# Optimization experiments

Measured on AMD Instinct MI355X. Metric: run time of the kernel, lower is better.

The kernel has to match this reference:

```python
import jax, jax.numpy as jnp
import numpy as np

N_HEAD = 8
N_HB_TERM = 3


def setup_inputs() -> dict:
    key = jax.random.key(0)
    ks = jax.random.split(key, 6)
    B, N, C, T = 8, 4096, 512, 4096
    s = 0.02  # weight init scale
    return {
        "x": jax.random.normal(ks[0], (B, N, C), jnp.float32),
        "y": jax.random.normal(ks[1], (N_HB_TERM, B, T, C), jnp.float32),
        "Wq": jax.random.normal(ks[2], (C, C), jnp.float32) * s,
        "bq": jnp.zeros((C,), jnp.float32),
        "Wk": jax.random.normal(ks[3], (N_HB_TERM, C, C), jnp.float32) * s,
        "bk": jnp.zeros((N_HB_TERM, C), jnp.float32),
        "Wv": jax.random.normal(ks[4], (N_HB_TERM, C, C), jnp.float32) * s,
        "bv": jnp.zeros((N_HB_TERM, C), jnp.float32),
        "Wp": jax.random.normal(ks[5], (C, C), jnp.float32) * s,
        "bp": jnp.zeros((C,), jnp.float32),
    }


def _heads(t, B, T, H, d):
    # (B, T, C) -> (B, H, T, d)
    return t.reshape(B, T, H, d).transpose(0, 2, 1, 3)


def reference(x, y, Wq, bq, Wk, bk, Wv, bv, Wp, bp):
    B, N, C = x.shape
    H = N_HEAD
    d = C // H
    # query projection + softmax feature map over head dim
    q = _heads(x @ Wq.T + bq, B, N, H, d)          # (B,H,N,d)
    q = jax.nn.softmax(q, axis=-1)
    out = q  # faithful to original: out initialized to q
    for i in range(N_HB_TERM):
        yi = y[i]                                   # (B,T,C)
        T = yi.shape[1]
        k = _heads(yi @ Wk[i].T + bk[i], B, T, H, d)
        v = _heads(yi @ Wv[i].T + bv[i], B, T, H, d)
        k = jax.nn.softmax(k, axis=-1)
        k_cumsum = k.sum(axis=-2, keepdims=True)    # (B,H,1,d)
        D_inv = 1.0 / (q * k_cumsum).sum(axis=-1, keepdims=True)  # (B,H,N,1)
        ctx = jnp.einsum('bhtd,bhte->bhde', k, v)   # (B,H,d,d) small context
        out = out + jnp.einsum('bhnd,bhde->bhne', q, ctx) * D_inv
    out = out.transpose(0, 2, 1, 3).reshape(B, N, C)  # b h n d -> b n (h d)
    return out @ Wp.T + bp
```

## Files before the change

kernel.cpp:

```cpp
#include <hip/hip_runtime.h>


#define B_  8
#define N_  4096
#define C_  512
#define T_  4096
#define H_  8
#define M_  (B_*N_)

typedef __bf16 bf16_8 __attribute__((ext_vector_type(8)));
typedef __bf16 bf16_4 __attribute__((ext_vector_type(4)));
typedef float  f32_4  __attribute__((ext_vector_type(4)));

__device__ __forceinline__ unsigned short f2bf(float f) {
  unsigned u = __float_as_uint(f);
  unsigned r = 0x7FFFu + ((u >> 16) & 1u);
  return (unsigned short)((u + r) >> 16);
}
__device__ __forceinline__ unsigned pack2(float lo, float hi) {
  return (unsigned)f2bf(lo) | ((unsigned)f2bf(hi) << 16);
}

__device__ __forceinline__ void gload16(const void* g, void* l) {
  __builtin_amdgcn_global_load_lds(
      (const __attribute__((address_space(1))) unsigned int*)g,
      (__attribute__((address_space(3))) unsigned int*)l, 16, 0, 0);
}

__device__ __forceinline__ bf16_8 cvt8(float4 a, float4 b) {
  bf16_8 v;
  v[0]=(__bf16)a.x; v[1]=(__bf16)a.y; v[2]=(__bf16)a.z; v[3]=(__bf16)a.w;
  v[4]=(__bf16)b.x; v[5]=(__bf16)b.y; v[6]=(__bf16)b.z; v[7]=(__bf16)b.w;
  return v;
}

__global__ __launch_bounds__(256) void cvt_all(
    const float* __restrict__ Wq, const float* __restrict__ Wk,
    const float* __restrict__ Wv, const float* __restrict__ Wp,
    const float* __restrict__ y,
    unsigned short* __restrict__ wb,
    unsigned short* __restrict__ yb)
{
  const size_t WCC = (size_t)C_*C_;
  const float* src; unsigned short* dst; long n8;
  switch (blockIdx.y) {
    case 0: src = Wq; dst = wb;         n8 = WCC/8;          break;
    case 1: src = Wk; dst = wb + WCC;   n8 = 3*WCC/8;        break;
    case 2: src = Wv; dst = wb + 4*WCC; n8 = 3*WCC/8;        break;
    case 3: src = Wp; dst = wb + 7*WCC; n8 = WCC/8;          break;
    default: src = y; dst = yb;         n8 = (long)3*M_*C_/8; break;
  }
  long i = (long)blockIdx.x * blockDim.x + threadIdx.x;
  long stride = (long)gridDim.x * blockDim.x;
  for (; i < n8; i += stride) {
    float4 a = ((const float4*)src)[2*i];
    float4 b = ((const float4*)src)[2*i + 1];
    uint4 o;
    o.x = pack2(a.x, a.y); o.y = pack2(a.z, a.w);
    o.z = pack2(b.x, b.y); o.w = pack2(b.z, b.w);
    ((uint4*)dst)[i] = o;
  }
}

__global__ __launch_bounds__(256, 2) void gemm_final(
    const unsigned short* __restrict__ A,
    const unsigned short* __restrict__ Bw,
    const float* __restrict__ bias,
    float* __restrict__ Cf)
{
  __shared__ char smem[65536];
  const int tid = threadIdx.x, lane = tid & 63, wid = tid >> 6;
  const int wr = wid >> 1, wc = wid & 1;
  const int l15 = lane & 15, l16 = lane >> 4;
  const size_t row0 = (size_t)blockIdx.x * 128;
  const int col0 = blockIdx.y * 128;

  f32_4 acc[4][4] = {};

  auto stage = [&](int k0, int bsel) {
#pragma unroll
    for (int j = 0; j < 4; ++j) {
      int cc = j*256 + tid, row = cc >> 3, s = cc & 7;
      gload16(A + (row0 + row)*512 + k0 + ((s ^ (row & 7)) << 3),
              smem + bsel*16384 + (size_t)(j*256 + wid*64)*16);
      gload16(Bw + (size_t)(col0 + row)*512 + k0 + ((s ^ (row & 7)) << 3),
              smem + 32768 + bsel*16384 + (size_t)(j*256 + wid*64)*16);
    }
  };

  stage(0, 0);
  __syncthreads();
  for (int t = 0; t < 8; ++t) {
    int cur = t & 1;
    if (t < 7) stage((t+1)*64, cur ^ 1);
    const unsigned short* sA = (const unsigned short*)(smem + cur*16384);
    const unsigned short* sB = (const unsigned short*)(smem + 32768 + cur*16384);
#pragma unroll
    for (int kk = 0; kk < 64; kk += 32) {
      bf16_8 af[4], bfr[4];
#pragma unroll
      for (int mi = 0; mi < 4; ++mi) {
        int r = wr*64 + mi*16 + l15;
        int ch = (kk >> 3) + l16;
        af[mi] = *(const bf16_8*)&sA[r*64 + ((ch ^ (r & 7)) << 3)];
      }
#pragma unroll
      for (int ni = 0; ni < 4; ++ni) {
        int r = wc*64 + ni*16 + l15;
        int ch = (kk >> 3) + l16;
        bfr[ni] = *(const bf16_8*)&sB[r*64 + ((ch ^ (r & 7)) << 3)];
      }
#pragma unroll
      for (int mi = 0; mi < 4; ++mi)
#pragma unroll
        for (int ni = 0; ni < 4; ++ni)
          acc[mi][ni] = __builtin_amdgcn_mfma_f32_16x16x32_bf16(af[mi], bfr[ni], acc[mi][ni], 0, 0, 0);
    }
    __syncthreads();
  }

#pragma unroll
  for (int mi = 0; mi < 4; ++mi) {
    int rb = wr*64 + mi*16 + l16*4;
#pragma unroll
    for (int ni = 0; ni < 4; ++ni) {
      int col = col0 + wc*64 + ni*16 + l15;
      float bv = bias[col];
#pragma unroll
      for (int jj = 0; jj < 4; ++jj)
        Cf[(row0 + rb + jj)*512 + col] = acc[mi][ni][jj] + bv;
    }
  }
}

__global__ __launch_bounds__(256, 2) void mega_kernel(
    const float* __restrict__ xf,
    const unsigned short* __restrict__ wq_b, const float* __restrict__ bq,
    unsigned short* __restrict__ qb,
    const unsigned short* __restrict__ yb_all,
    const unsigned short* __restrict__ wk_all,
    const unsigned short* __restrict__ wv_all,
    const float* __restrict__ bk_all, const float* __restrict__ bv_all,
    float* __restrict__ part, float* __restrict__ kcp)
{
  __shared__ char smem[65536];
  const int tid = threadIdx.x, lane = tid & 63, wid = tid >> 6;
  const int wr = wid >> 1, wc = wid & 1;
  const int l15 = lane & 15, l16 = lane >> 4;
  const int z = blockIdx.z;

  if (z < 2) {
    const int qidx = z*512 + blockIdx.x;
    const size_t row0 = (size_t)(qidx & 255) * 128;
    const int col0 = (qidx >> 8) * 128;

    f32_4 acc[4][4] = {};
    float4 ra[4][2];

    auto load_a = [&](int k0) {
#pragma unroll
      for (int j = 0; j < 4; ++j) {
        int cc = j*256 + tid, row = cc >> 3, s = cc & 7;
        const float* src = xf + (row0 + row)*512 + k0 + s*8;
        ra[j][0] = *(const float4*)src;
        ra[j][1] = *(const float4*)(src + 4);
      }
    };
    auto write_a = [&](int bsel) {
      unsigned short* dst = (unsigned short*)smem;
#pragma unroll
      for (int j = 0; j < 4; ++j) {
        int cc = j*256 + tid, row = cc >> 3, s = cc & 7;
        *(bf16_8*)&dst[bsel*8192 + row*64 + ((s ^ (row & 7)) << 3)] = cvt8(ra[j][0], ra[j][1]);
      }
    };
    auto stage_b = [&](int k0, int bsel) {
#pragma unroll
      for (int j = 0; j < 4; ++j) {
        int cc = j*256 + tid, row = cc >> 3, s = cc & 7;
        gload16(wq_b + (size_t)(col0 + row)*512 + k0 + ((s ^ (row & 7)) << 3),
                smem + 32768 + bsel*16384 + (size_t)(j*256 + wid*64)*16);
      }
    };

    load_a(0); stage_b(0, 0); write_a(0);
    __syncthreads();
    for (int t = 0; t < 8; ++t) {
      int cur = t & 1;
      if (t < 7) { load_a((t+1)*64); stage_b((t+1)*64, cur ^ 1); }
      const unsigned short* sA = (const unsigned short*)(smem + cur*16384);
      const unsigned short* sB = (const unsigned short*)(smem + 32768 + cur*16384);
#pragma unroll
      for (int kk = 0; kk < 64; kk += 32) {
        bf16_8 af[4], bfr[4];
#pragma unroll
        for (int mi = 0; mi < 4; ++mi) {
          int r = wr*64 + mi*16 + l15;
          int ch = (kk >> 3) + l16;
          af[mi] = *(const bf16_8*)&sA[r*64 + ((ch ^ (r & 7)) << 3)];
        }
#pragma unroll
        for (int ni = 0; ni < 4; ++ni) {
          int r = wc*64 + ni*16 + l15;
          int ch = (kk >> 3) + l16;
          bfr[ni] = *(const bf16_8*)&sB[r*64 + ((ch ^ (r & 7)) << 3)];
        }
#pragma unroll
        for (int mi = 0; mi < 4; ++mi)
#pragma unroll
          for (int ni = 0; ni < 4; ++ni)
            acc[mi][ni] = __builtin_amdgcn_mfma_f32_16x16x32_bf16(af[mi], bfr[ni], acc[mi][ni], 0, 0, 0);
      }
      if (t < 7) write_a(cur ^ 1);
      __syncthreads();
    }

    float bvv[4];
#pragma unroll
    for (int ni = 0; ni < 4; ++ni) bvv[ni] = bq[col0 + wc*64 + ni*16 + l15];
    unsigned short* sE = (unsigned short*)smem;
#pragma unroll
    for (int mi = 0; mi < 4; ++mi) {
#pragma unroll
      for (int jj = 0; jj < 4; ++jj) {
        float x[4];
        float s = 0.f;
#pragma unroll
        for (int ni = 0; ni < 4; ++ni) {
          x[ni] = __expf(acc[mi][ni][jj] + bvv[ni]);
          s += x[ni];
        }
#pragma unroll
        for (int o = 8; o; o >>= 1) s += __shfl_xor(s, o);
        float inv = 1.0f / s;
        int r = wr*64 + mi*16 + l16*4 + jj;
#pragma unroll
        for (int ni = 0; ni < 4; ++ni) {
          __bf16 h = (__bf16)(x[ni] * inv);
          sE[r*136 + wc*64 + ni*16 + l15] = *(unsigned short*)&h;
        }
      }
    }
    __syncthreads();
    int r = tid >> 1, seg = tid & 1;
    unsigned short* orow = qb + (row0 + r)*512 + col0 + seg*64;
#pragma unroll
    for (int u = 0; u < 8; ++u)
      *(uint4*)(orow + u*8) = *(const uint4*)&sE[r*136 + seg*64 + u*8];
    return;
  }

  unsigned short* sKT = (unsigned short*)smem;
  unsigned short* sVT = (unsigned short*)(smem + 17408);

  const int gx = blockIdx.x, i = z - 2;
  const int h = gx >> 6, bx = gx & 63;
  const int b = bx >> 3, sub = bx & 7;
  const int bh = b*8 + h;

  const unsigned short* yb = yb_all + (size_t)i*M_*512;
  const unsigned short* Wk_b = wk_all + (size_t)i*512*512 + (size_t)h*64*512;
  const unsigned short* Wv_b = wv_all + (size_t)i*512*512 + (size_t)h*64*512;
  const float* bk = bk_all + i*512 + h*64;
  const float* bv = bv_all + i*512 + h*64;

  f32_4 cacc[2][2] = {};
  float kcp_r[4] = {0.f, 0.f, 0.f, 0.f};

  for (int chunk = 0; chunk < 4; ++chunk) {
    const size_t row0 = (size_t)bx*512 + chunk*128;
    f32_4 acc[4][4] = {};

    auto stage = [&](int k0, int bsel) {
#pragma unroll
      for (int j = 0; j < 4; ++j) {
        int cc = j*256 + tid, row = cc >> 3, s = cc & 7;
        gload16(yb + (row0 + row)*512 + k0 + ((s ^ (row & 7)) << 3),
                smem + bsel*16384 + (size_t)(j*256 + wid*64)*16);
        const unsigned short* wsrc = (j < 2)
            ? Wk_b + (size_t)row*512
            : Wv_b + (size_t)(row - 64)*512;
        gload16(wsrc + k0 + ((s ^ (row & 7)) << 3),
                smem + 32768 + bsel*16384 + (size_t)(j*256 + wid*64)*16);
      }
    };

    stage(0, 0);
    __syncthreads();
    for (int t = 0; t < 8; ++t) {
      int cur = t & 1;
      if (t < 7) stage((t+1)*64, cur ^ 1);
      const unsigned short* sA = (const unsigned short*)(smem + cur*16384);
      const unsigned short* sB = (const unsigned short*)(smem + 32768 + cur*16384);
#pragma unroll
      for (int kk = 0; kk < 64; kk += 32) {
        bf16_8 af[4], bfr[4];
#pragma unroll
        for (int mi = 0; mi < 4; ++mi) {
          int r = wr*64 + mi*16 + l15;
          int ch = (kk >> 3) + l16;
          af[mi] = *(const bf16_8*)&sA[r*64 + ((ch ^ (r & 7)) << 3)];
        }
#pragma unroll
        for (int ni = 0; ni < 4; ++ni) {
          int r = wc*64 + ni*16 + l15;
          int ch = (kk >> 3) + l16;
          bfr[ni] = *(const bf16_8*)&sB[r*64 + ((ch ^ (r & 7)) << 3)];
        }
#pragma unroll
        for (int mi = 0; mi < 4; ++mi)
#pragma unroll
          for (int ni = 0; ni < 4; ++ni)
            acc[mi][ni] = __builtin_amdgcn_mfma_f32_16x16x32_bf16(af[mi], bfr[ni], acc[mi][ni], 0, 0, 0);
      }
      __syncthreads();
    }

    if (wc == 0) {
      float bkv[4];
#pragma unroll
      for (int ni = 0; ni < 4; ++ni) bkv[ni] = bk[ni*16 + l15];
#pragma unroll
      for (int mi = 0; mi < 4; ++mi) {
        float kv[4][4];
#pragma unroll
        for (int jj = 0; jj < 4; ++jj) {
          float s = 0.f;
#pragma unroll
          for (int ni = 0; ni < 4; ++ni) {
            kv[jj][ni] = __expf(acc[mi][ni][jj] + bkv[ni]);
            s += kv[jj][ni];
          }
#pragma unroll
          for (int o = 8; o; o >>= 1) s += __shfl_xor(s, o);
          float inv = 1.0f / s;
#pragma unroll
          for (int ni = 0; ni < 4; ++ni) kv[jj][ni] *= inv;
        }
        int r0 = wr*64 + mi*16 + l16*4;
#pragma unroll
        for (int ni = 0; ni < 4; ++ni) {
          kcp_r[ni] += (kv[0][ni] + kv[1][ni]) + (kv[2][ni] + kv[3][ni]);
          bf16_4 p;
#pragma unroll
          for (int jj = 0; jj < 4; ++jj) p[jj] = (__bf16)kv[jj][ni];
          *(bf16_4*)&sKT[(ni*16 + l15)*136 + r0] = p;
        }
      }
    } else {
      float bvv[4];
#pragma unroll
      for (int ni = 0; ni < 4; ++ni) bvv[ni] = bv[ni*16 + l15];
#pragma unroll
      for (int mi = 0; mi < 4; ++mi) {
        int r0 = wr*64 + mi*16 + l16*4;
#pragma unroll
        for (int ni = 0; ni < 4; ++ni) {
          bf16_4 p;
#pragma unroll
          for (int jj = 0; jj < 4; ++jj) p[jj] = (__bf16)(acc[mi][ni][jj] + bvv[ni]);
          *(bf16_4*)&sVT[(ni*16 + l15)*136 + r0] = p;
        }
      }
    }
    __syncthreads();

#pragma unroll
    for (int ks = 0; ks < 4; ++ks) {
      bf16_8 a2[2], b2[2];
#pragma unroll
      for (int mi = 0; mi < 2; ++mi)
        a2[mi] = *(const bf16_8*)&sKT[(wr*32 + mi*16 + l15)*136 + ks*32 + l16*8];
#pragma unroll
      for (int ni = 0; ni < 2; ++ni)
        b2[ni] = *(const bf16_8*)&sVT[(wc*32 + ni*16 + l15)*136 + ks*32 + l16*8];
#pragma unroll
      for (int mi = 0; mi < 2; ++mi)
#pragma unroll
        for (int ni = 0; ni < 2; ++ni)
          cacc[mi][ni] = __builtin_amdgcn_mfma_f32_16x16x32_bf16(a2[mi], b2[ni], cacc[mi][ni], 0, 0, 0);
    }
    __syncthreads();
  }

  const size_t slot = (size_t)(i*64 + bh)*8 + sub;
  if (wc == 0) {
#pragma unroll
    for (int ni = 0; ni < 4; ++ni) {
      float s = kcp_r[ni];
      s += __shfl_xor(s, 16);
      s += __shfl_xor(s, 32);
      if (l16 == 0) kcp[(slot*2 + wr)*64 + ni*16 + l15] = s;
    }
  }
  float* pb = part + slot*4096;
#pragma unroll
  for (int mi = 0; mi < 2; ++mi)
#pragma unroll
    for (int ni = 0; ni < 2; ++ni) {
      int e0 = wr*32 + mi*16 + l16*4;
      int dv = wc*32 + ni*16 + l15;
      *(f32_4*)&pb[dv*64 + e0] = cacc[mi][ni];
    }
}

__global__ __launch_bounds__(256) void ctx_reduce(
    const float* __restrict__ part,
    const float* __restrict__ kcp,
    float* __restrict__ ctxT,
    float* __restrict__ kc)
{
  int g = blockIdx.x;
  const float* p = part + (size_t)g*8*4096;
  float* o = ctxT + (size_t)g*4096;
#pragma unroll
  for (int jj = 0; jj < 4; ++jj) {
    int j = (jj*256 + threadIdx.x)*4;
    f32_4 s = {};
#pragma unroll
    for (int r = 0; r < 8; ++r) {
      f32_4 v = *(const f32_4*)&p[(size_t)r*4096 + j];
      s[0] += v[0]; s[1] += v[1]; s[2] += v[2]; s[3] += v[3];
    }
    *(f32_4*)&o[j] = s;
  }
  if (threadIdx.x < 64) {
    const float* pk = kcp + (size_t)g*16*64;
    float s = 0.f;
#pragma unroll
    for (int r = 0; r < 16; ++r) s += pk[r*64 + threadIdx.x];
    kc[(size_t)g*64 + threadIdx.x] = s;
  }
}

__global__ __launch_bounds__(256) void combine2(
    const unsigned short* __restrict__ qb,
    const float* __restrict__ ctxT,
    const float* __restrict__ kc,
    unsigned short* __restrict__ outp)
{
  __shared__ unsigned short sQ[128*64];
  __shared__ unsigned short sB[208*72];
  __shared__ float sS[128*3];
  const int tid = threadIdx.x, lane = tid & 63, wid = tid >> 6;
  const int l15 = lane & 15, l16 = lane >> 4;
  const int bh = blockIdx.y, b = bh >> 3, h = bh & 7;
  const int n0 = blockIdx.x * 128;
  const size_t qbase = ((size_t)b*N_ + n0)*C_ + h*64;

#pragma unroll
  for (int j = 0; j < 4; ++j) {
    int c = j*256 + tid;
    int row = c >> 3, c8 = c & 7;
    gload16(qb + qbase + (size_t)row*C_ + ((c8 ^ (row & 7)) << 3),
            sQ + (size_t)(j*256 + wid*64)*8);
  }
  for (int f = tid; f < 208*64; f += 256) {
    int col = f >> 6, e = f & 63;
    float val = 0.f;
    if (col < 192)
      val = ctxT[(((size_t)(col >> 6)*64 + bh)*64 + (col & 63))*64 + e];
    else if (col < 195)
      val = kc[((size_t)(col - 192)*64 + bh)*64 + e];
    __bf16 hv = (__bf16)val;
    sB[col*72 + e] = *(unsigned short*)&hv;
  }
  __syncthreads();

  f32_4 acc[2][13] = {};
#pragma unroll
  for (int ks = 0; ks < 2; ++ks) {
    bf16_8 af[2];
#pragma unroll
    for (int mi = 0; mi < 2; ++mi) {
      int r = wid*32 + mi*16 + l15;
      int ch = ks*4 + l16;
      af[mi] = *(const bf16_8*)&sQ[r*64 + ((ch ^ (r & 7)) << 3)];
    }
#pragma unroll
    for (int ni = 0; ni < 13; ++ni) {
      bf16_8 bfr = *(const bf16_8*)&sB[(ni*16 + l15)*72 + ks*32 + l16*8];
#pragma unroll
      for (int mi = 0; mi < 2; ++mi)
        acc[mi][ni] = __builtin_amdgcn_mfma_f32_16x16x32_bf16(af[mi], bfr, acc[mi][ni], 0, 0, 0);
    }
  }

  if (l15 < 3) {
#pragma unroll
    for (int mi = 0; mi < 2; ++mi)
#pragma unroll
      for (int jj = 0; jj < 4; ++jj)
        sS[(wid*32 + mi*16 + l16*4 + jj)*3 + l15] = acc[mi][12][jj];
  }
  __syncthreads();

#pragma unroll
  for (int mi = 0; mi < 2; ++mi) {
#pragma unroll
    for (int jj = 0; jj < 4; ++jj) {
      int r = wid*32 + mi*16 + l16*4 + jj;
      float inv[3];
#pragma unroll
      for (int i = 0; i < 3; ++i) inv[i] = 1.0f / sS[r*3 + i];
#pragma unroll
      for (int ni = 0; ni < 4; ++ni) {
        int dv = ni*16 + l15;
        unsigned short qh = sQ[r*64 + ((((dv >> 3) ^ (r & 7))) << 3) + (dv & 7)];
        float val = __uint_as_float(((unsigned)qh) << 16);
#pragma unroll
        for (int i = 0; i < 3; ++i) val += acc[mi][i*4 + ni][jj] * inv[i];
        __bf16 hv = (__bf16)val;
        outp[qbase + (size_t)r*C_ + dv] = *(unsigned short*)&hv;
      }
    }
  }
}

extern "C" void kernel_launch(void* const* d_in, const int* in_sizes, int n_in,
                              void* d_out, int out_size, void* d_ws, size_t ws_size,
                              hipStream_t stream)
{
  const float* x  = (const float*)d_in[0];
  const float* y  = (const float*)d_in[1];
  const float* Wq = (const float*)d_in[2];
  const float* bq = (const float*)d_in[3];
  const float* Wk = (const float*)d_in[4];
  const float* bk = (const float*)d_in[5];
  const float* Wv = (const float*)d_in[6];
  const float* bv = (const float*)d_in[7];
  const float* Wp = (const float*)d_in[8];
  const float* bp = (const float*)d_in[9];
  float* out = (float*)d_out;
  char* ws = (char*)d_ws;

  const size_t SZ_BF = (size_t)M_ * C_ * 2;
  const size_t WCC   = (size_t)C_ * C_;

  unsigned short* yb   = (unsigned short*)(ws);
  unsigned short* qb   = (unsigned short*)(ws + 3*SZ_BF);
  unsigned short* kb   = (unsigned short*)(ws + 4*SZ_BF);
  unsigned short* wb   = (unsigned short*)(ws + 5*SZ_BF);
  unsigned short* wq_b = wb;
  unsigned short* wk_b = wb + WCC;
  unsigned short* wv_b = wb + 4*WCC;
  unsigned short* wp_b = wb + 7*WCC;
  float* ctxT = (float*)(wb + 8*WCC);
  float* kc   = ctxT + (size_t)3*64*64*64;

  float* part  = (float*)kb;
  float* kcpar = part + (size_t)192*8*4096;

  cvt_all<<<dim3(2048, 5), 256, 0, stream>>>(Wq, Wk, Wv, Wp, y, wb, yb);

  mega_kernel<<<dim3(512, 1, 5), 256, 0, stream>>>(
      x, wq_b, bq, qb, yb, wk_b, wv_b, bk, bv, part, kcpar);
  ctx_reduce<<<192, 256, 0, stream>>>(part, kcpar, ctxT, kc);

  combine2<<<dim3(32, 64), 256, 0, stream>>>(qb, ctxT, kc, kb);
  gemm_final<<<dim3(M_/128, 4), 256, 0, stream>>>(kb, wp_b, bp, out);
}
```

Baseline: 364.7 us.

## Overlap y bf16 conversion with Q projection, split K/V context kernel

Moves the large fp32-to-bf16 conversion of y out of the up-front conversion kernel and interleaves it, on alternate blocks, with the Q projection/softmax GEMM in a new kernel. The K/V context work becomes its own kernel launched afterwards. The goal is to hide the bandwidth-bound y conversion behind compute-bound Q GEMM blocks, leaving only the small weight conversion serialized. The cost is an extra kernel launch, and the K/V blocks can no longer run concurrently with the Q blocks.

Measured after the change: 376.4 us. 1.03x slower.

```diff
diff --git a/kernel.cpp b/kernel.cpp
--- a/kernel.cpp
+++ b/kernel.cpp
@@ -34,65 +34,94 @@
   return v;
 }
 
-__global__ __launch_bounds__(256) void cvt_all(
+__global__ __launch_bounds__(256) void cvt_weights(
     const float* __restrict__ Wq, const float* __restrict__ Wk,
     const float* __restrict__ Wv, const float* __restrict__ Wp,
-    const float* __restrict__ y,
-    unsigned short* __restrict__ wb,
-    unsigned short* __restrict__ yb)
+    unsigned short* __restrict__ wb)
 {
   const size_t WCC = (size_t)C_*C_;
-  const float* src; unsigned short* dst; long n8;
+  const float* src; unsigned short* dst; long n4;
   switch (blockIdx.y) {
-    case 0: src = Wq; dst = wb;         n8 = WCC/8;          break;
-    case 1: src = Wk; dst = wb + WCC;   n8 = 3*WCC/8;        break;
-    case 2: src = Wv; dst = wb + 4*WCC; n8 = 3*WCC/8;        break;
-    case 3: src = Wp; dst = wb + 7*WCC; n8 = WCC/8;          break;
-    default: src = y; dst = yb;         n8 = (long)3*M_*C_/8; break;
+    case 0: src = Wq; dst = wb;         n4 = WCC/4;   break;
+    case 1: src = Wk; dst = wb + WCC;   n4 = 3*WCC/4; break;
+    case 2: src = Wv; dst = wb + 4*WCC; n4 = 3*WCC/4; break;
+    default:src = Wp; dst = wb + 7*WCC; n4 = WCC/4;   break;
   }
   long i = (long)blockIdx.x * blockDim.x + threadIdx.x;
   long stride = (long)gridDim.x * blockDim.x;
-  for (; i < n8; i += stride) {
-    float4 a = ((const float4*)src)[2*i];
-    float4 b = ((const float4*)src)[2*i + 1];
-    uint4 o;
-    o.x = pack2(a.x, a.y); o.y = pack2(a.z, a.w);
-    o.z = pack2(b.x, b.y); o.w = pack2(b.z, b.w);
-    ((uint4*)dst)[i] = o;
-  }
-}
-
-__global__ __launch_bounds__(256, 2) void gemm_final(
-    const unsigned short* __restrict__ A,
-    const unsigned short* __restrict__ Bw,
-    const float* __restrict__ bias,
-    float* __restrict__ Cf)
+  for (; i < n4; i += stride) {
+    float4 v = ((const float4*)src)[i];
+    ushort4 o;
+    o.x = f2bf(v.x); o.y = f2bf(v.y); o.z = f2bf(v.z); o.w = f2bf(v.w);
+    ((ushort4*)dst)[i] = o;
+  }
+}
+
+__global__ __launch_bounds__(256, 2) void qcvt_kernel(
+    const float* __restrict__ xf,
+    const unsigned short* __restrict__ wq_b, const float* __restrict__ bq,
+    unsigned short* __restrict__ qb,
+    const float* __restrict__ y, unsigned short* __restrict__ yb)
 {
   __shared__ char smem[65536];
   const int tid = threadIdx.x, lane = tid & 63, wid = tid >> 6;
   const int wr = wid >> 1, wc = wid & 1;
   const int l15 = lane & 15, l16 = lane >> 4;
-  const size_t row0 = (size_t)blockIdx.x * 128;
-  const int col0 = blockIdx.y * 128;
+  const int flat = blockIdx.x;
+
+  if (flat & 1) {
+    const long n8 = (long)3*M_*C_/8;
+    const long per = n8 / 1024;
+    const long beg = (long)(flat >> 1) * per;
+    for (long i = beg + tid; i < beg + per; i += 256) {
+      float4 a = ((const float4*)y)[2*i];
+      float4 b = ((const float4*)y)[2*i + 1];
+      uint4 o;
+      o.x = pack2(a.x, a.y); o.y = pack2(a.z, a.w);
+      o.z = pack2(b.x, b.y); o.w = pack2(b.z, b.w);
+      ((uint4*)yb)[i] = o;
+    }
+    return;
+  }
+
+  const int qidx = flat >> 1;
+  const size_t row0 = (size_t)(qidx & 255) * 128;
+  const int col0 = (qidx >> 8) * 128;
 
   f32_4 acc[4][4] = {};
-
-  auto stage = [&](int k0, int bsel) {
+  float4 ra[4][2];
+
+  auto load_a = [&](int k0) {
 #pragma unroll
     for (int j = 0; j < 4; ++j) {
       int cc = j*256 + tid, row = cc >> 3, s = cc & 7;
-      gload16(A + (row0 + row)*512 + k0 + ((s ^ (row & 7)) << 3),
-              smem + bsel*16384 + (size_t)(j*256 + wid*64)*16);
-      gload16(Bw + (size_t)(col0 + row)*512 + k0 + ((s ^ (row & 7)) << 3),
+      const float* src = xf + (row0 + row)*512 + k0 + s*8;
+      ra[j][0] = *(const float4*)src;
+      ra[j][1] = *(const float4*)(src + 4);
+    }
+  };
+  auto write_a = [&](int bsel) {
+    unsigned short* dst = (unsigned short*)smem;
+#pragma unroll
+    for (int j = 0; j < 4; ++j) {
+      int cc = j*256 + tid, row = cc >> 3, s = cc & 7;
+      *(bf16_8*)&dst[bsel*8192 + row*64 + ((s ^ (row & 7)) << 3)] = cvt8(ra[j][0], ra[j][1]);
+    }
+  };
+  auto stage_b = [&](int k0, int bsel) {
+#pragma unroll
+    for (int j = 0; j < 4; ++j) {
+      int cc = j*256 + tid, row = cc >> 3, s = cc & 7;
+      gload16(wq_b + (size_t)(col0 + row)*512 + k0 + ((s ^ (row & 7)) << 3),
               smem + 32768 + bsel*16384 + (size_t)(j*256 + wid*64)*16);
     }
   };
 
-  stage(0, 0);
+  load_a(0); stage_b(0, 0); write_a(0);
   __syncthreads();
   for (int t = 0; t < 8; ++t) {
     int cur = t & 1;
-    if (t < 7) stage((t+1)*64, cur ^ 1);
+    if (t < 7) { load_a((t+1)*64); stage_b((t+1)*64, cur ^ 1); }
     const unsigned short* sA = (const unsigned short*)(smem + cur*16384);
     const unsigned short* sB = (const unsigned short*)(smem + 32768 + cur*16384);
 #pragma unroll
@@ -116,27 +145,45 @@
         for (int ni = 0; ni < 4; ++ni)
           acc[mi][ni] = __builtin_amdgcn_mfma_f32_16x16x32_bf16(af[mi], bfr[ni], acc[mi][ni], 0, 0, 0);
     }
+    if (t < 7) write_a(cur ^ 1);
     __syncthreads();
   }
 
+  float bvv[4];
+#pragma unroll
+  for (int ni = 0; ni < 4; ++ni) bvv[ni] = bq[col0 + wc*64 + ni*16 + l15];
+  unsigned short* sE = (unsigned short*)smem;
 #pragma unroll
   for (int mi = 0; mi < 4; ++mi) {
-    int rb = wr*64 + mi*16 + l16*4;
-#pragma unroll
-    for (int ni = 0; ni < 4; ++ni) {
-      int col = col0 + wc*64 + ni*16 + l15;
-      float bv = bias[col];
-#pragma unroll
-      for (int jj = 0; jj < 4; ++jj)
-        Cf[(row0 + rb + jj)*512 + col] = acc[mi][ni][jj] + bv;
-    }
-  }
-}
-
-__global__ __launch_bounds__(256, 2) void mega_kernel(
-    const float* __restrict__ xf,
-    const unsigned short* __restrict__ wq_b, const float* __restrict__ bq,
-    unsigned short* __restrict__ qb,
+#pragma unroll
+    for (int jj = 0; jj < 4; ++jj) {
+      float x[4];
+      float s = 0.f;
+#pragma unroll
+      for (int ni = 0; ni < 4; ++ni) {
+        x[ni] = __expf(acc[mi][ni][jj] + bvv[ni]);
+        s += x[ni];
+      }
+#pragma unroll
+      for (int o = 8; o; o >>= 1) s += __shfl_xor(s, o);
+      float inv = 1.0f / s;
+      int r = wr*64 + mi*16 + l16*4 + jj;
+#pragma unroll
+      for (int ni = 0; ni < 4; ++ni) {
+        __bf16 h = (__bf16)(x[ni] * inv);
+        sE[r*136 + wc*64 + ni*16 + l15] = *(unsigned short*)&h;
+      }
+    }
+  }
+  __syncthreads();
+  int r = tid >> 1, seg = tid & 1;
+  unsigned short* orow = qb + (row0 + r)*512 + col0 + seg*64;
+#pragma unroll
+  for (int u = 0; u < 8; ++u)
+    *(uint4*)(orow + u*8) = *(const uint4*)&sE[r*136 + seg*64 + u*8];
+}
+
+__global__ __launch_bounds__(256, 2) void kvctx_kernel(
     const unsigned short* __restrict__ yb_all,
     const unsigned short* __restrict__ wk_all,
     const unsigned short* __restrict__ wv_all,
@@ -144,116 +191,13 @@
     float* __restrict__ part, float* __restrict__ kcp)
 {
   __shared__ char smem[65536];
+  unsigned short* sKT = (unsigned short*)smem;
+  unsigned short* sVT = (unsigned short*)(smem + 17408);
+
   const int tid = threadIdx.x, lane = tid & 63, wid = tid >> 6;
   const int wr = wid >> 1, wc = wid & 1;
   const int l15 = lane & 15, l16 = lane >> 4;
-  const int z = blockIdx.z;
-
-  if (z < 2) {
-    const int qidx = z*512 + blockIdx.x;
-    const size_t row0 = (size_t)(qidx & 255) * 128;
-    const int col0 = (qidx >> 8) * 128;
-
-    f32_4 acc[4][4] = {};
-    float4 ra[4][2];
-
-    auto load_a = [&](int k0) {
-#pragma unroll
-      for (int j = 0; j < 4; ++j) {
-        int cc = j*256 + tid, row = cc >> 3, s = cc & 7;
-        const float* src = xf + (row0 + row)*512 + k0 + s*8;
-        ra[j][0] = *(const float4*)src;
-        ra[j][1] = *(const float4*)(src + 4);
-      }
-    };
-    auto write_a = [&](int bsel) {
-      unsigned short* dst = (unsigned short*)smem;
-#pragma unroll
-      for (int j = 0; j < 4; ++j) {
-        int cc = j*256 + tid, row = cc >> 3, s = cc & 7;
-        *(bf16_8*)&dst[bsel*8192 + row*64 + ((s ^ (row & 7)) << 3)] = cvt8(ra[j][0], ra[j][1]);
-      }
-    };
-    auto stage_b = [&](int k0, int bsel) {
-#pragma unroll
-      for (int j = 0; j < 4; ++j) {
-        int cc = j*256 + tid, row = cc >> 3, s = cc & 7;
-        gload16(wq_b + (size_t)(col0 + row)*512 + k0 + ((s ^ (row & 7)) << 3),
-                smem + 32768 + bsel*16384 + (size_t)(j*256 + wid*64)*16);
-      }
-    };
-
-    load_a(0); stage_b(0, 0); write_a(0);
-    __syncthreads();
-    for (int t = 0; t < 8; ++t) {
-      int cur = t & 1;
-      if (t < 7) { load_a((t+1)*64); stage_b((t+1)*64, cur ^ 1); }
-      const unsigned short* sA = (const unsigned short*)(smem + cur*16384);
-      const unsigned short* sB = (const unsigned short*)(smem + 32768 + cur*16384);
-#pragma unroll
-      for (int kk = 0; kk < 64; kk += 32) {
-        bf16_8 af[4], bfr[4];
-#pragma unroll
-        for (int mi = 0; mi < 4; ++mi) {
-          int r = wr*64 + mi*16 + l15;
-          int ch = (kk >> 3) + l16;
-          af[mi] = *(const bf16_8*)&sA[r*64 + ((ch ^ (r & 7)) << 3)];
-        }
-#pragma unroll
-        for (int ni = 0; ni < 4; ++ni) {
-          int r = wc*64 + ni*16 + l15;
-          int ch = (kk >> 3) + l16;
-          bfr[ni] = *(const bf16_8*)&sB[r*64 + ((ch ^ (r & 7)) << 3)];
-        }
-#pragma unroll
-        for (int mi = 0; mi < 4; ++mi)
-#pragma unroll
-          for (int ni = 0; ni < 4; ++ni)
-            acc[mi][ni] = __builtin_amdgcn_mfma_f32_16x16x32_bf16(af[mi], bfr[ni], acc[mi][ni], 0, 0, 0);
-      }
-      if (t < 7) write_a(cur ^ 1);
-      __syncthreads();
-    }
-
-    float bvv[4];
-#pragma unroll
-    for (int ni = 0; ni < 4; ++ni) bvv[ni] = bq[col0 + wc*64 + ni*16 + l15];
-    unsigned short* sE = (unsigned short*)smem;
-#pragma unroll
-    for (int mi = 0; mi < 4; ++mi) {
-#pragma unroll
-      for (int jj = 0; jj < 4; ++jj) {
-        float x[4];
-        float s = 0.f;
-#pragma unroll
-        for (int ni = 0; ni < 4; ++ni) {
-          x[ni] = __expf(acc[mi][ni][jj] + bvv[ni]);
-          s += x[ni];
-        }
-#pragma unroll
-        for (int o = 8; o; o >>= 1) s += __shfl_xor(s, o);
-        float inv = 1.0f / s;
-        int r = wr*64 + mi*16 + l16*4 + jj;
-#pragma unroll
-        for (int ni = 0; ni < 4; ++ni) {
-          __bf16 h = (__bf16)(x[ni] * inv);
-          sE[r*136 + wc*64 + ni*16 + l15] = *(unsigned short*)&h;
-        }
-      }
-    }
-    __syncthreads();
-    int r = tid >> 1, seg = tid & 1;
-    unsigned short* orow = qb + (row0 + r)*512 + col0 + seg*64;
-#pragma unroll
-    for (int u = 0; u < 8; ++u)
-      *(uint4*)(orow + u*8) = *(const uint4*)&sE[r*136 + seg*64 + u*8];
-    return;
-  }
-
-  unsigned short* sKT = (unsigned short*)smem;
-  unsigned short* sVT = (unsigned short*)(smem + 17408);
-
-  const int gx = blockIdx.x, i = z - 2;
+  const int gx = blockIdx.x, i = blockIdx.z;
   const int h = gx >> 6, bx = gx & 63;
   const int b = bx >> 3, sub = bx & 7;
   const int bh = b*8 + h;
@@ -513,6 +457,77 @@
         __bf16 hv = (__bf16)val;
         outp[qbase + (size_t)r*C_ + dv] = *(unsigned short*)&hv;
       }
+    }
+  }
+}
+
+__global__ __launch_bounds__(256, 2) void gemm_final(
+    const unsigned short* __restrict__ A,
+    const unsigned short* __restrict__ Bw,
+    const float* __restrict__ bias,
+    float* __restrict__ Cf)
+{
+  __shared__ char smem[65536];
+  const int tid = threadIdx.x, lane = tid & 63, wid = tid >> 6;
+  const int wr = wid >> 1, wc = wid & 1;
+  const int l15 = lane & 15, l16 = lane >> 4;
+  const size_t row0 = (size_t)blockIdx.x * 128;
+  const int col0 = blockIdx.y * 128;
+
+  f32_4 acc[4][4] = {};
+
+  auto stage = [&](int k0, int bsel) {
+#pragma unroll
+    for (int j = 0; j < 4; ++j) {
+      int cc = j*256 + tid, row = cc >> 3, s = cc & 7;
+      gload16(A + (row0 + row)*512 + k0 + ((s ^ (row & 7)) << 3),
+              smem + bsel*16384 + (size_t)(j*256 + wid*64)*16);
+      gload16(Bw + (size_t)(col0 + row)*512 + k0 + ((s ^ (row & 7)) << 3),
+              smem + 32768 + bsel*16384 + (size_t)(j*256 + wid*64)*16);
+    }
+  };
+
+  stage(0, 0);
+  __syncthreads();
+  for (int t = 0; t < 8; ++t) {
+    int cur = t & 1;
+    if (t < 7) stage((t+1)*64, cur ^ 1);
+    const unsigned short* sA = (const unsigned short*)(smem + cur*16384);
+    const unsigned short* sB = (const unsigned short*)(smem + 32768 + cur*16384);
+#pragma unroll
+    for (int kk = 0; kk < 64; kk += 32) {
+      bf16_8 af[4], bfr[4];
+#pragma unroll
+      for (int mi = 0; mi < 4; ++mi) {
+        int r = wr*64 + mi*16 + l15;
+        int ch = (kk >> 3) + l16;
+        af[mi] = *(const bf16_8*)&sA[r*64 + ((ch ^ (r & 7)) << 3)];
+      }
+#pragma unroll
+      for (int ni = 0; ni < 4; ++ni) {
+        int r = wc*64 + ni*16 + l15;
+        int ch = (kk >> 3) + l16;
+        bfr[ni] = *(const bf16_8*)&sB[r*64 + ((ch ^ (r & 7)) << 3)];
+      }
+#pragma unroll
+      for (int mi = 0; mi < 4; ++mi)
+#pragma unroll
+        for (int ni = 0; ni < 4; ++ni)
+          acc[mi][ni] = __builtin_amdgcn_mfma_f32_16x16x32_bf16(af[mi], bfr[ni], acc[mi][ni], 0, 0, 0);
+    }
+    __syncthreads();
+  }
+
+#pragma unroll
+  for (int mi = 0; mi < 4; ++mi) {
+    int rb = wr*64 + mi*16 + l16*4;
+#pragma unroll
+    for (int ni = 0; ni < 4; ++ni) {
+      int col = col0 + wc*64 + ni*16 + l15;
+      float bv = bias[col];
+#pragma unroll
+      for (int jj = 0; jj < 4; ++jj)
+        Cf[(row0 + rb + jj)*512 + col] = acc[mi][ni][jj] + bv;
     }
   }
 }
@@ -551,10 +566,12 @@
   float* part  = (float*)kb;
   float* kcpar = part + (size_t)192*8*4096;
 
-  cvt_all<<<dim3(2048, 5), 256, 0, stream>>>(Wq, Wk, Wv, Wp, y, wb, yb);
-
-  mega_kernel<<<dim3(512, 1, 5), 256, 0, stream>>>(
-      x, wq_b, bq, qb, yb, wk_b, wv_b, bk, bv, part, kcpar);
+  cvt_weights<<<dim3(128, 4), 256, 0, stream>>>(Wq, Wk, Wv, Wp, wb);
+
+  qcvt_kernel<<<2048, 256, 0, stream>>>(x, wq_b, bq, qb, y, yb);
+
+  kvctx_kernel<<<dim3(512, 1, 3), 256, 0, stream>>>(
+      yb, wk_b, wv_b, bk, bv, part, kcpar);
   ctx_reduce<<<192, 256, 0, stream>>>(part, kcpar, ctxT, kc);
 
   combine2<<<dim3(32, 64), 256, 0, stream>>>(qb, ctxT, kc, kb);
```
